# Optimization experiments

Measured on AMD Instinct MI355X. Metric: run time of the kernel, lower is better.

Reference implementation:

```python
import jax, jax.numpy as jnp
import numpy as np

B, T, F, U = 256, 512, 64, 128

def setup_inputs() -> dict:
    key = jax.random.key(0)
    ks = jax.random.split(key, 8)
    def ortho(k, n):
        a = jax.random.normal(k, (n, n), dtype=jnp.float32)
        q, _ = jnp.linalg.qr(a)
        return q.astype(jnp.float32)
    return {
        "x": jax.random.normal(ks[0], (B, T, F), dtype=jnp.float32),
        "m": jax.random.uniform(ks[1], (B, T, F), dtype=jnp.float32),
        "delta_t": jax.random.uniform(ks[2], (B, T), dtype=jnp.float32),
        "W_z": jax.random.normal(ks[3], (F, U), dtype=jnp.float32) * 0.08,
        "U_z": ortho(ks[4], U),
        "b_z": jnp.zeros((U,), jnp.float32),
        "W_r": jax.random.normal(ks[5], (F, U), dtype=jnp.float32) * 0.08,
        "U_r": ortho(ks[6], U),
        "b_r": jnp.zeros((U,), jnp.float32),
        "W_h": jax.random.normal(ks[7], (F, U), dtype=jnp.float32) * 0.08,
        "U_h": ortho(jax.random.fold_in(key, 99), U),
        "b_h": jnp.zeros((U,), jnp.float32),
        "gamma_x_decay": jnp.ones((F,), jnp.float32),
        "gamma_h_decay": jnp.ones((U,), jnp.float32),
        "mean_imputation": jnp.zeros((F,), jnp.float32),
    }

def reference(x, m, delta_t, W_z, U_z, b_z, W_r, U_r, b_r, W_h, U_h, b_h,
              gamma_x_decay, gamma_h_decay, mean_imputation):
    # delta_t: [B,T] -> [B,T,1]
    dt = delta_t[..., None]
    # input-side decay + imputation (no recurrence -> fully vectorized)
    gamma_x = jnp.exp(-jnp.maximum(0.0, gamma_x_decay) * dt)          # [B,T,F]
    x_dec = m * x + (1.0 - m) * (gamma_x * x + (1.0 - gamma_x) * mean_imputation)
    gamma_h = jnp.exp(-jnp.maximum(0.0, gamma_h_decay) * dt)          # [B,T,U]
    # precompute input projections for all timesteps
    xz = jnp.einsum('btf,fu->btu', x_dec, W_z) + b_z
    xr = jnp.einsum('btf,fu->btu', x_dec, W_r) + b_r
    xh = jnp.einsum('btf,fu->btu', x_dec, W_h) + b_h

    def step(h, inp):
        gz, az, ar, ah = inp            # gamma_h_t [B,U], projected inputs [B,U]
        h_dec = gz * h
        z = jax.nn.sigmoid(az + h_dec @ U_z)
        r = jax.nn.sigmoid(ar + h_dec @ U_r)
        h_hat = jnp.tanh(ah + (r * h_dec) @ U_h)
        h_new = (1.0 - z) * h_dec + z * h_hat
        return h_new, h_new

    h0 = jnp.zeros((x.shape[0], U_z.shape[0]), x.dtype)
    xs = (jnp.swapaxes(gamma_h, 0, 1), jnp.swapaxes(xz, 0, 1),
          jnp.swapaxes(xr, 0, 1), jnp.swapaxes(xh, 0, 1))
    _, hs = jax.lax.scan(step, h0, xs)  # [T,B,U]
    return jnp.swapaxes(hs, 0, 1)       # [B,T,U]
```

## Files before the change

### kernel.cpp

```cpp
#include <hip/hip_runtime.h>

#define B_ 256
#define T_ 512
#define F_ 64
#define U_ 128
#define PSTRIDE 132

typedef _Float16 h2v __attribute__((ext_vector_type(2)));
union U32H2 { unsigned u; h2v h; };

__device__ __forceinline__ float fdot2u(unsigned a, unsigned b, float c) {
#if __has_builtin(__builtin_amdgcn_fdot2)
  U32H2 x, y; x.u = a; y.u = b;
  return __builtin_amdgcn_fdot2(x.h, y.h, c, false);
#else
  U32H2 x, y; x.u = a; y.u = b;
  c = fmaf((float)x.h[0], (float)y.h[0], c);
  return fmaf((float)x.h[1], (float)y.h[1], c);
#endif
}

__device__ __forceinline__ unsigned packh2(float a, float b) {
  U32H2 r; r.h[0] = (_Float16)a; r.h[1] = (_Float16)b; return r.u;
}

__device__ __forceinline__ float red8(float v) {
  int t;
  t = __builtin_amdgcn_update_dpp(0, __float_as_int(v), 0xB1, 0xF, 0xF, true);
  v += __int_as_float(t);
  t = __builtin_amdgcn_update_dpp(0, __float_as_int(v), 0x4E, 0xF, 0xF, true);
  v += __int_as_float(t);
  t = __builtin_amdgcn_update_dpp(0, __float_as_int(v), 0x141, 0xF, 0xF, true);
  v += __int_as_float(t);
  return v;
}

__device__ __forceinline__ float fast_sig(float x) {
  return __builtin_amdgcn_rcpf(1.0f + __expf(-x));
}
__device__ __forceinline__ float fast_tanh(float x) {
  return fmaf(-2.0f, __builtin_amdgcn_rcpf(1.0f + __expf(2.0f * x)), 1.0f);
}

__global__ __launch_bounds__(512, 2) void grud_kernel(
    const float* __restrict__ x, const float* __restrict__ m,
    const float* __restrict__ delta_t,
    const float* __restrict__ Wz, const float* __restrict__ Uz, const float* __restrict__ bz,
    const float* __restrict__ Wr, const float* __restrict__ Ur, const float* __restrict__ br,
    const float* __restrict__ Wh, const float* __restrict__ Uh, const float* __restrict__ bh,
    const float* __restrict__ gxd, const float* __restrict__ ghd,
    const float* __restrict__ mi,
    float* __restrict__ out)
{
  const int tid = threadIdx.x;
  const int b   = blockIdx.x;
  const int kq  = tid & 7;
  const int ow  = tid >> 3;
  const int u0  = 2 * ow;

  __shared__ float s_mem[16896];
  float*  const s_pool = s_mem;
  float*  const s_gh   = s_mem;
  float*  const s_hist = s_mem + 4096;
  ushort* const s_x16  = (ushort*)(s_mem + 8192);
  __shared__ __align__(16) ushort s_hd16[U_];
  __shared__ __align__(16) ushort s_rh16[U_];
  __shared__ float s_dt[40];
  __shared__ float s_negghd[U_];

  unsigned uz0[8], uz1[8], ur0[8], ur1[8], uh0[8], uh1[8];
  unsigned wz0[4], wz1[4], wr0[4], wr1[4], wh0[4], wh1[4];

#define STAGE_MAT(SRC, ROWS)                                      \
  {                                                               \
    const float4* g4 = (const float4*)(SRC);                      \
    _Pragma("unroll") for (int i = 0; i < (ROWS) / 16; ++i) {     \
      const int e = tid + i * 512;                                \
      const int r = e >> 5, c = (e & 31) << 2;                    \
      *(float4*)(s_pool + r * PSTRIDE + c) = g4[e];               \
    }                                                             \
    __syncthreads();                                              \
  }

#define GATHER_U(D0, D1)                                          \
  _Pragma("unroll") for (int j = 0; j < 8; ++j) {                 \
    const int k = 16 * kq + 2 * j;                                \
    D0[j] = packh2(s_pool[k * PSTRIDE + u0],                      \
                   s_pool[(k + 1) * PSTRIDE + u0]);               \
    D1[j] = packh2(s_pool[k * PSTRIDE + u0 + 1],                  \
                   s_pool[(k + 1) * PSTRIDE + u0 + 1]);           \
  }                                                               \
  __syncthreads();

#define GATHER_W(D0, D1)                                          \
  _Pragma("unroll") for (int j = 0; j < 4; ++j) {                 \
    const int f = 8 * kq + 2 * j;                                 \
    D0[j] = packh2(s_pool[f * PSTRIDE + u0],                      \
                   s_pool[(f + 1) * PSTRIDE + u0]);               \
    D1[j] = packh2(s_pool[f * PSTRIDE + u0 + 1],                  \
                   s_pool[(f + 1) * PSTRIDE + u0 + 1]);           \
  }                                                               \
  __syncthreads();

  STAGE_MAT(Uz, 128) GATHER_U(uz0, uz1)
  STAGE_MAT(Ur, 128) GATHER_U(ur0, ur1)
  STAGE_MAT(Uh, 128) GATHER_U(uh0, uh1)
  STAGE_MAT(Wz, 64)  GATHER_W(wz0, wz1)
  STAGE_MAT(Wr, 64)  GATHER_W(wr0, wr1)
  STAGE_MAT(Wh, 64)  GATHER_W(wh0, wh1)

  const float2 bz2 = ((const float2*)bz)[ow];
  const float2 br2 = ((const float2*)br)[ow];
  const float2 bh2 = ((const float2*)bh)[ow];

  if (tid < U_) {
    s_negghd[tid] = -fmaxf(ghd[tid], 0.0f);
    ((ushort*)s_hd16)[tid] = 0;
  }

  float hd0 = 0.0f, hd1 = 0.0f;
  float z0 = 0.0f, z1 = 0.0f;

  for (int t0 = 0; t0 < T_; t0 += 32) {
    if (tid < 33) {
      const int t = t0 + tid;
      s_dt[tid] = (t < T_) ? delta_t[b * T_ + t] : 0.0f;
    }
    __syncthreads();

#pragma unroll
    for (int i = 0; i < 8; ++i) {
      const int flat = tid + i * 512;
      const int tcc = flat >> 7, u = flat & 127;
      s_gh[flat] = __expf(s_negghd[u] * s_dt[tcc + 1]);
    }
    {
      const int idx0 = tid * 4;
      const int tt = idx0 >> 6, f0 = idx0 & 63;
      const float dtv = s_dt[tt];
      const float4 xv  = *(const float4*)(x  + (size_t)(b * T_ + t0 + tt) * F_ + f0);
      const float4 mv  = *(const float4*)(m  + (size_t)(b * T_ + t0 + tt) * F_ + f0);
      const float4 gv  = *(const float4*)(gxd + f0);
      const float4 miv = *(const float4*)(mi  + f0);
      float gx, d0, d1, d2, d3;
      gx = __expf(-fmaxf(gv.x, 0.0f) * dtv);
      d0 = mv.x * xv.x + (1.0f - mv.x) * (gx * xv.x + (1.0f - gx) * miv.x);
      gx = __expf(-fmaxf(gv.y, 0.0f) * dtv);
      d1 = mv.y * xv.y + (1.0f - mv.y) * (gx * xv.y + (1.0f - gx) * miv.y);
      gx = __expf(-fmaxf(gv.z, 0.0f) * dtv);
      d2 = mv.z * xv.z + (1.0f - mv.z) * (gx * xv.z + (1.0f - gx) * miv.z);
      gx = __expf(-fmaxf(gv.w, 0.0f) * dtv);
      d3 = mv.w * xv.w + (1.0f - mv.w) * (gx * xv.w + (1.0f - gx) * miv.w);
      uint2 px; px.x = packh2(d0, d1); px.y = packh2(d2, d3);
      *(uint2*)(s_x16 + idx0) = px;
    }
    __syncthreads();

#pragma unroll 4
    for (int tc = 0; tc < 32; ++tc) {
      const uint4 ha = *(const uint4*)(s_hd16 + 16 * kq);
      const uint4 hb = *(const uint4*)(s_hd16 + 16 * kq + 8);
      const uint4 xa = *(const uint4*)(s_x16 + tc * F_ + 8 * kq);

      float az0 = 0.f, az1 = 0.f, ar0 = 0.f, ar1 = 0.f, ah0 = 0.f, ah1 = 0.f;
      az0 = fdot2u(ha.x, uz0[0], az0); az0 = fdot2u(ha.y, uz0[1], az0);
      az0 = fdot2u(ha.z, uz0[2], az0); az0 = fdot2u(ha.w, uz0[3], az0);
      az0 = fdot2u(hb.x, uz0[4], az0); az0 = fdot2u(hb.y, uz0[5], az0);
      az0 = fdot2u(hb.z, uz0[6], az0); az0 = fdot2u(hb.w, uz0[7], az0);
      az1 = fdot2u(ha.x, uz1[0], az1); az1 = fdot2u(ha.y, uz1[1], az1);
      az1 = fdot2u(ha.z, uz1[2], az1); az1 = fdot2u(ha.w, uz1[3], az1);
      az1 = fdot2u(hb.x, uz1[4], az1); az1 = fdot2u(hb.y, uz1[5], az1);
      az1 = fdot2u(hb.z, uz1[6], az1); az1 = fdot2u(hb.w, uz1[7], az1);
      ar0 = fdot2u(ha.x, ur0[0], ar0); ar0 = fdot2u(ha.y, ur0[1], ar0);
      ar0 = fdot2u(ha.z, ur0[2], ar0); ar0 = fdot2u(ha.w, ur0[3], ar0);
      ar0 = fdot2u(hb.x, ur0[4], ar0); ar0 = fdot2u(hb.y, ur0[5], ar0);
      ar0 = fdot2u(hb.z, ur0[6], ar0); ar0 = fdot2u(hb.w, ur0[7], ar0);
      ar1 = fdot2u(ha.x, ur1[0], ar1); ar1 = fdot2u(ha.y, ur1[1], ar1);
      ar1 = fdot2u(ha.z, ur1[2], ar1); ar1 = fdot2u(ha.w, ur1[3], ar1);
      ar1 = fdot2u(hb.x, ur1[4], ar1); ar1 = fdot2u(hb.y, ur1[5], ar1);
      ar1 = fdot2u(hb.z, ur1[6], ar1); ar1 = fdot2u(hb.w, ur1[7], ar1);

      az0 = fdot2u(xa.x, wz0[0], az0); az0 = fdot2u(xa.y, wz0[1], az0);
      az0 = fdot2u(xa.z, wz0[2], az0); az0 = fdot2u(xa.w, wz0[3], az0);
      az1 = fdot2u(xa.x, wz1[0], az1); az1 = fdot2u(xa.y, wz1[1], az1);
      az1 = fdot2u(xa.z, wz1[2], az1); az1 = fdot2u(xa.w, wz1[3], az1);
      ar0 = fdot2u(xa.x, wr0[0], ar0); ar0 = fdot2u(xa.y, wr0[1], ar0);
      ar0 = fdot2u(xa.z, wr0[2], ar0); ar0 = fdot2u(xa.w, wr0[3], ar0);
      ar1 = fdot2u(xa.x, wr1[0], ar1); ar1 = fdot2u(xa.y, wr1[1], ar1);
      ar1 = fdot2u(xa.z, wr1[2], ar1); ar1 = fdot2u(xa.w, wr1[3], ar1);
      ah0 = fdot2u(xa.x, wh0[0], ah0); ah0 = fdot2u(xa.y, wh0[1], ah0);
      ah0 = fdot2u(xa.z, wh0[2], ah0); ah0 = fdot2u(xa.w, wh0[3], ah0);
      ah1 = fdot2u(xa.x, wh1[0], ah1); ah1 = fdot2u(xa.y, wh1[1], ah1);
      ah1 = fdot2u(xa.z, wh1[2], ah1); ah1 = fdot2u(xa.w, wh1[3], ah1);

      az0 = red8(az0); az1 = red8(az1);
      ar0 = red8(ar0); ar1 = red8(ar1);
      z0 = fast_sig(az0 + bz2.x);
      z1 = fast_sig(az1 + bz2.y);
      const float r0 = fast_sig(ar0 + br2.x);
      const float r1 = fast_sig(ar1 + br2.y);
      if (kq == 0) {
        ((unsigned*)s_rh16)[ow] = packh2(r0 * hd0, r1 * hd1);
      }
      __syncthreads();

      const uint4 ra = *(const uint4*)(s_rh16 + 16 * kq);
      const uint4 rb = *(const uint4*)(s_rh16 + 16 * kq + 8);
      ah0 = fdot2u(ra.x, uh0[0], ah0); ah0 = fdot2u(ra.y, uh0[1], ah0);
      ah0 = fdot2u(ra.z, uh0[2], ah0); ah0 = fdot2u(ra.w, uh0[3], ah0);
      ah0 = fdot2u(rb.x, uh0[4], ah0); ah0 = fdot2u(rb.y, uh0[5], ah0);
      ah0 = fdot2u(rb.z, uh0[6], ah0); ah0 = fdot2u(rb.w, uh0[7], ah0);
      ah1 = fdot2u(ra.x, uh1[0], ah1); ah1 = fdot2u(ra.y, uh1[1], ah1);
      ah1 = fdot2u(ra.z, uh1[2], ah1); ah1 = fdot2u(ra.w, uh1[3], ah1);
      ah1 = fdot2u(rb.x, uh1[4], ah1); ah1 = fdot2u(rb.y, uh1[5], ah1);
      ah1 = fdot2u(rb.z, uh1[6], ah1); ah1 = fdot2u(rb.w, uh1[7], ah1);
      ah0 = red8(ah0); ah1 = red8(ah1);
      if (kq == 0) {
        const float hh0 = fast_tanh(ah0 + bh2.x);
        const float hh1 = fast_tanh(ah1 + bh2.y);
        const float hn0 = fmaf(z0, hh0 - hd0, hd0);
        const float hn1 = fmaf(z1, hh1 - hd1, hd1);
        ((float2*)s_hist)[tc * 64 + ow] = make_float2(hn0, hn1);
        const float2 gh = ((const float2*)s_gh)[tc * 64 + ow];
        hd0 = gh.x * hn0;
        hd1 = gh.y * hn1;
        ((unsigned*)s_hd16)[ow] = packh2(hd0, hd1);
      }
      __syncthreads();
    }

    {
      const float4* h4p = (const float4*)s_hist;
      float4* o4 = (float4*)(out + (size_t)(b * T_ + t0) * U_);
      o4[tid]       = h4p[tid];
      o4[tid + 512] = h4p[tid + 512];
    }
    __syncthreads();
  }
}

extern "C" void kernel_launch(void* const* d_in, const int* in_sizes, int n_in,
                              void* d_out, int out_size, void* d_ws, size_t ws_size,
                              hipStream_t stream) {
  const float* x   = (const float*)d_in[0];
  const float* m   = (const float*)d_in[1];
  const float* dt  = (const float*)d_in[2];
  const float* Wz  = (const float*)d_in[3];
  const float* Uz  = (const float*)d_in[4];
  const float* bz  = (const float*)d_in[5];
  const float* Wr  = (const float*)d_in[6];
  const float* Ur  = (const float*)d_in[7];
  const float* br  = (const float*)d_in[8];
  const float* Wh  = (const float*)d_in[9];
  const float* Uh  = (const float*)d_in[10];
  const float* bh  = (const float*)d_in[11];
  const float* gxd = (const float*)d_in[12];
  const float* ghd = (const float*)d_in[13];
  const float* mi  = (const float*)d_in[14];

  grud_kernel<<<dim3(B_), dim3(512), 0, stream>>>(
      x, m, dt, Wz, Uz, bz, Wr, Ur, br, Wh, Uh, bh, gxd, ghd, mi, (float*)d_out);
}
```

Measured before the change: 408.5 us.

## Specialize wavefront teams per gate and pipeline input projections one step ahead

Replaces the 8-way split-K layout, where each output pair was reduced across lanes with DPP, with four 128-thread teams. Each thread holds one full weight column in registers. Team 0 computes z, team 1 computes r, team 2 computes h_hat and the state update, and team 3 computes the next step's input projections into a double-buffered shared array. This removes the cross-lane reductions and the redundant work of computing input projections in every thread. Output is now written per step straight from registers instead of via a staged shared history. The cost is that each thread does a full 128-long serial dot product, teams sit idle in alternate phases, and register pressure rises (96 packed weights per thread, with the launch-bounds occupancy hint removed).

New measurement: 443.3 us. 8.5% more time.

```diff
diff --git a/kernel.cpp b/kernel.cpp
--- a/kernel.cpp
+++ b/kernel.cpp
@@ -9,32 +9,15 @@
 typedef _Float16 h2v __attribute__((ext_vector_type(2)));
 union U32H2 { unsigned u; h2v h; };
 
-__device__ __forceinline__ float fdot2u(unsigned a, unsigned b, float c) {
-#if __has_builtin(__builtin_amdgcn_fdot2)
+__device__ __forceinline__ float fdot2(unsigned a, unsigned b, float c) {
   U32H2 x, y; x.u = a; y.u = b;
   return __builtin_amdgcn_fdot2(x.h, y.h, c, false);
-#else
-  U32H2 x, y; x.u = a; y.u = b;
-  c = fmaf((float)x.h[0], (float)y.h[0], c);
-  return fmaf((float)x.h[1], (float)y.h[1], c);
-#endif
 }
 
 __device__ __forceinline__ unsigned packh2(float a, float b) {
   U32H2 r; r.h[0] = (_Float16)a; r.h[1] = (_Float16)b; return r.u;
 }
 
-__device__ __forceinline__ float red8(float v) {
-  int t;
-  t = __builtin_amdgcn_update_dpp(0, __float_as_int(v), 0xB1, 0xF, 0xF, true);
-  v += __int_as_float(t);
-  t = __builtin_amdgcn_update_dpp(0, __float_as_int(v), 0x4E, 0xF, 0xF, true);
-  v += __int_as_float(t);
-  t = __builtin_amdgcn_update_dpp(0, __float_as_int(v), 0x141, 0xF, 0xF, true);
-  v += __int_as_float(t);
-  return v;
-}
-
 __device__ __forceinline__ float fast_sig(float x) {
   return __builtin_amdgcn_rcpf(1.0f + __expf(-x));
 }
@@ -42,7 +25,7 @@
   return fmaf(-2.0f, __builtin_amdgcn_rcpf(1.0f + __expf(2.0f * x)), 1.0f);
 }
 
-__global__ __launch_bounds__(512, 2) void grud_kernel(
+__global__ __launch_bounds__(512) void grud_kernel(
     const float* __restrict__ x, const float* __restrict__ m,
     const float* __restrict__ delta_t,
     const float* __restrict__ Wz, const float* __restrict__ Uz, const float* __restrict__ bz,
@@ -52,24 +35,21 @@
     const float* __restrict__ mi,
     float* __restrict__ out)
 {
-  const int tid = threadIdx.x;
-  const int b   = blockIdx.x;
-  const int kq  = tid & 7;
-  const int ow  = tid >> 3;
-  const int u0  = 2 * ow;
-
-  __shared__ float s_mem[16896];
+  const int tid  = threadIdx.x;
+  const int b    = blockIdx.x;
+  const int team = tid >> 7;
+  const int uu   = tid & 127;
+
+  __shared__ float s_mem[U_ * PSTRIDE];
   float*  const s_pool = s_mem;
-  float*  const s_gh   = s_mem;
-  float*  const s_hist = s_mem + 4096;
-  ushort* const s_x16  = (ushort*)(s_mem + 8192);
+  float*  const s_zf   = s_mem;
+  float*  const s_ax   = s_mem + 128;
+  ushort* const s_x16h = (ushort*)(s_mem + 896);
   __shared__ __align__(16) ushort s_hd16[U_];
   __shared__ __align__(16) ushort s_rh16[U_];
   __shared__ float s_dt[40];
-  __shared__ float s_negghd[U_];
-
-  unsigned uz0[8], uz1[8], ur0[8], ur1[8], uh0[8], uh1[8];
-  unsigned wz0[4], wz1[4], wr0[4], wr1[4], wh0[4], wh1[4];
+
+  unsigned wcol[96];
 
 #define STAGE_MAT(SRC, ROWS)                                      \
   {                                                               \
@@ -82,62 +62,67 @@
     __syncthreads();                                              \
   }
 
-#define GATHER_U(D0, D1)                                          \
-  _Pragma("unroll") for (int j = 0; j < 8; ++j) {                 \
-    const int k = 16 * kq + 2 * j;                                \
-    D0[j] = packh2(s_pool[k * PSTRIDE + u0],                      \
-                   s_pool[(k + 1) * PSTRIDE + u0]);               \
-    D1[j] = packh2(s_pool[k * PSTRIDE + u0 + 1],                  \
-                   s_pool[(k + 1) * PSTRIDE + u0 + 1]);           \
-  }                                                               \
-  __syncthreads();
-
-#define GATHER_W(D0, D1)                                          \
-  _Pragma("unroll") for (int j = 0; j < 4; ++j) {                 \
-    const int f = 8 * kq + 2 * j;                                 \
-    D0[j] = packh2(s_pool[f * PSTRIDE + u0],                      \
-                   s_pool[(f + 1) * PSTRIDE + u0]);               \
-    D1[j] = packh2(s_pool[f * PSTRIDE + u0 + 1],                  \
-                   s_pool[(f + 1) * PSTRIDE + u0 + 1]);           \
-  }                                                               \
-  __syncthreads();
-
-  STAGE_MAT(Uz, 128) GATHER_U(uz0, uz1)
-  STAGE_MAT(Ur, 128) GATHER_U(ur0, ur1)
-  STAGE_MAT(Uh, 128) GATHER_U(uh0, uh1)
-  STAGE_MAT(Wz, 64)  GATHER_W(wz0, wz1)
-  STAGE_MAT(Wr, 64)  GATHER_W(wr0, wr1)
-  STAGE_MAT(Wh, 64)  GATHER_W(wh0, wh1)
-
-  const float2 bz2 = ((const float2*)bz)[ow];
-  const float2 br2 = ((const float2*)br)[ow];
-  const float2 bh2 = ((const float2*)bh)[ow];
-
-  if (tid < U_) {
-    s_negghd[tid] = -fmaxf(ghd[tid], 0.0f);
-    ((ushort*)s_hd16)[tid] = 0;
-  }
-
-  float hd0 = 0.0f, hd1 = 0.0f;
-  float z0 = 0.0f, z1 = 0.0f;
+  STAGE_MAT(Uz, 128)
+  if (team == 0) {
+#pragma unroll
+    for (int j = 0; j < 64; ++j)
+      wcol[j] = packh2(s_pool[(2 * j) * PSTRIDE + uu], s_pool[(2 * j + 1) * PSTRIDE + uu]);
+  }
+  __syncthreads();
+  STAGE_MAT(Ur, 128)
+  if (team == 1) {
+#pragma unroll
+    for (int j = 0; j < 64; ++j)
+      wcol[j] = packh2(s_pool[(2 * j) * PSTRIDE + uu], s_pool[(2 * j + 1) * PSTRIDE + uu]);
+  }
+  __syncthreads();
+  STAGE_MAT(Uh, 128)
+  if (team == 2) {
+#pragma unroll
+    for (int j = 0; j < 64; ++j)
+      wcol[j] = packh2(s_pool[(2 * j) * PSTRIDE + uu], s_pool[(2 * j + 1) * PSTRIDE + uu]);
+  }
+  __syncthreads();
+  STAGE_MAT(Wz, 64)
+  if (team == 3) {
+#pragma unroll
+    for (int j = 0; j < 32; ++j)
+      wcol[j] = packh2(s_pool[(2 * j) * PSTRIDE + uu], s_pool[(2 * j + 1) * PSTRIDE + uu]);
+  }
+  __syncthreads();
+  STAGE_MAT(Wr, 64)
+  if (team == 3) {
+#pragma unroll
+    for (int j = 0; j < 32; ++j)
+      wcol[32 + j] = packh2(s_pool[(2 * j) * PSTRIDE + uu], s_pool[(2 * j + 1) * PSTRIDE + uu]);
+  }
+  __syncthreads();
+  STAGE_MAT(Wh, 64)
+  if (team == 3) {
+#pragma unroll
+    for (int j = 0; j < 32; ++j)
+      wcol[64 + j] = packh2(s_pool[(2 * j) * PSTRIDE + uu], s_pool[(2 * j + 1) * PSTRIDE + uu]);
+  }
+  __syncthreads();
+
+  float bzu = 0.f, bru = 0.f, bhu = 0.f;
+  float negg = 0.f, hd_reg = 0.f;
+  if (team == 3) { bzu = bz[uu]; bru = br[uu]; bhu = bh[uu]; }
+  if (team == 2) { negg = -fmaxf(ghd[uu], 0.0f); }
+  if (tid < U_) s_hd16[tid] = 0;
+
+  const uint4* const hd4 = (const uint4*)s_hd16;
+  const uint4* const rh4 = (const uint4*)s_rh16;
 
   for (int t0 = 0; t0 < T_; t0 += 32) {
     if (tid < 33) {
       const int t = t0 + tid;
       s_dt[tid] = (t < T_) ? delta_t[b * T_ + t] : 0.0f;
     }
-    __syncthreads();
-
-#pragma unroll
-    for (int i = 0; i < 8; ++i) {
-      const int flat = tid + i * 512;
-      const int tcc = flat >> 7, u = flat & 127;
-      s_gh[flat] = __expf(s_negghd[u] * s_dt[tcc + 1]);
-    }
     {
       const int idx0 = tid * 4;
       const int tt = idx0 >> 6, f0 = idx0 & 63;
-      const float dtv = s_dt[tt];
+      const float dtv = delta_t[b * T_ + t0 + tt];
       const float4 xv  = *(const float4*)(x  + (size_t)(b * T_ + t0 + tt) * F_ + f0);
       const float4 mv  = *(const float4*)(m  + (size_t)(b * T_ + t0 + tt) * F_ + f0);
       const float4 gv  = *(const float4*)(gxd + f0);
@@ -152,90 +137,120 @@
       gx = __expf(-fmaxf(gv.w, 0.0f) * dtv);
       d3 = mv.w * xv.w + (1.0f - mv.w) * (gx * xv.w + (1.0f - gx) * miv.w);
       uint2 px; px.x = packh2(d0, d1); px.y = packh2(d2, d3);
-      *(uint2*)(s_x16 + idx0) = px;
+      *(uint2*)(s_x16h + idx0) = px;
     }
     __syncthreads();
 
-#pragma unroll 4
+    if (team == 3) {
+      const uint4* xp = (const uint4*)s_x16h;
+      float a0 = bzu, a1 = bru, a2 = bhu;
+#pragma unroll
+      for (int q = 0; q < 8; ++q) {
+        const uint4 xq = xp[q];
+        a0 = fdot2(xq.x, wcol[4*q+0], a0); a0 = fdot2(xq.y, wcol[4*q+1], a0);
+        a0 = fdot2(xq.z, wcol[4*q+2], a0); a0 = fdot2(xq.w, wcol[4*q+3], a0);
+        a1 = fdot2(xq.x, wcol[32+4*q+0], a1); a1 = fdot2(xq.y, wcol[32+4*q+1], a1);
+        a1 = fdot2(xq.z, wcol[32+4*q+2], a1); a1 = fdot2(xq.w, wcol[32+4*q+3], a1);
+        a2 = fdot2(xq.x, wcol[64+4*q+0], a2); a2 = fdot2(xq.y, wcol[64+4*q+1], a2);
+        a2 = fdot2(xq.z, wcol[64+4*q+2], a2); a2 = fdot2(xq.w, wcol[64+4*q+3], a2);
+      }
+      s_ax[0 * 384 + 0 * 128 + uu] = a0;
+      s_ax[0 * 384 + 1 * 128 + uu] = a1;
+      s_ax[0 * 384 + 2 * 128 + uu] = a2;
+    }
+    __syncthreads();
+
+#pragma unroll 2
     for (int tc = 0; tc < 32; ++tc) {
-      const uint4 ha = *(const uint4*)(s_hd16 + 16 * kq);
-      const uint4 hb = *(const uint4*)(s_hd16 + 16 * kq + 8);
-      const uint4 xa = *(const uint4*)(s_x16 + tc * F_ + 8 * kq);
-
-      float az0 = 0.f, az1 = 0.f, ar0 = 0.f, ar1 = 0.f, ah0 = 0.f, ah1 = 0.f;
-      az0 = fdot2u(ha.x, uz0[0], az0); az0 = fdot2u(ha.y, uz0[1], az0);
-      az0 = fdot2u(ha.z, uz0[2], az0); az0 = fdot2u(ha.w, uz0[3], az0);
-      az0 = fdot2u(hb.x, uz0[4], az0); az0 = fdot2u(hb.y, uz0[5], az0);
-      az0 = fdot2u(hb.z, uz0[6], az0); az0 = fdot2u(hb.w, uz0[7], az0);
-      az1 = fdot2u(ha.x, uz1[0], az1); az1 = fdot2u(ha.y, uz1[1], az1);
-      az1 = fdot2u(ha.z, uz1[2], az1); az1 = fdot2u(ha.w, uz1[3], az1);
-      az1 = fdot2u(hb.x, uz1[4], az1); az1 = fdot2u(hb.y, uz1[5], az1);
-      az1 = fdot2u(hb.z, uz1[6], az1); az1 = fdot2u(hb.w, uz1[7], az1);
-      ar0 = fdot2u(ha.x, ur0[0], ar0); ar0 = fdot2u(ha.y, ur0[1], ar0);
-      ar0 = fdot2u(ha.z, ur0[2], ar0); ar0 = fdot2u(ha.w, ur0[3], ar0);
-      ar0 = fdot2u(hb.x, ur0[4], ar0); ar0 = fdot2u(hb.y, ur0[5], ar0);
-      ar0 = fdot2u(hb.z, ur0[6], ar0); ar0 = fdot2u(hb.w, ur0[7], ar0);
-      ar1 = fdot2u(ha.x, ur1[0], ar1); ar1 = fdot2u(ha.y, ur1[1], ar1);
-      ar1 = fdot2u(ha.z, ur1[2], ar1); ar1 = fdot2u(ha.w, ur1[3], ar1);
-      ar1 = fdot2u(hb.x, ur1[4], ar1); ar1 = fdot2u(hb.y, ur1[5], ar1);
-      ar1 = fdot2u(hb.z, ur1[6], ar1); ar1 = fdot2u(hb.w, ur1[7], ar1);
-
-      az0 = fdot2u(xa.x, wz0[0], az0); az0 = fdot2u(xa.y, wz0[1], az0);
-      az0 = fdot2u(xa.z, wz0[2], az0); az0 = fdot2u(xa.w, wz0[3], az0);
-      az1 = fdot2u(xa.x, wz1[0], az1); az1 = fdot2u(xa.y, wz1[1], az1);
-      az1 = fdot2u(xa.z, wz1[2], az1); az1 = fdot2u(xa.w, wz1[3], az1);
-      ar0 = fdot2u(xa.x, wr0[0], ar0); ar0 = fdot2u(xa.y, wr0[1], ar0);
-      ar0 = fdot2u(xa.z, wr0[2], ar0); ar0 = fdot2u(xa.w, wr0[3], ar0);
-      ar1 = fdot2u(xa.x, wr1[0], ar1); ar1 = fdot2u(xa.y, wr1[1], ar1);
-      ar1 = fdot2u(xa.z, wr1[2], ar1); ar1 = fdot2u(xa.w, wr1[3], ar1);
-      ah0 = fdot2u(xa.x, wh0[0], ah0); ah0 = fdot2u(xa.y, wh0[1], ah0);
-      ah0 = fdot2u(xa.z, wh0[2], ah0); ah0 = fdot2u(xa.w, wh0[3], ah0);
-      ah1 = fdot2u(xa.x, wh1[0], ah1); ah1 = fdot2u(xa.y, wh1[1], ah1);
-      ah1 = fdot2u(xa.z, wh1[2], ah1); ah1 = fdot2u(xa.w, wh1[3], ah1);
-
-      az0 = red8(az0); az1 = red8(az1);
-      ar0 = red8(ar0); ar1 = red8(ar1);
-      z0 = fast_sig(az0 + bz2.x);
-      z1 = fast_sig(az1 + bz2.y);
-      const float r0 = fast_sig(ar0 + br2.x);
-      const float r1 = fast_sig(ar1 + br2.y);
-      if (kq == 0) {
-        ((unsigned*)s_rh16)[ow] = packh2(r0 * hd0, r1 * hd1);
+      const int cur = tc & 1, nxt = cur ^ 1;
+
+      if (team == 0) {
+        float a0 = s_ax[cur * 384 + uu], a1 = 0.f, a2 = 0.f, a3 = 0.f;
+#pragma unroll
+        for (int q = 0; q < 4; ++q) {
+          const uint4 h0 = hd4[4*q+0], h1 = hd4[4*q+1], h2 = hd4[4*q+2], h3 = hd4[4*q+3];
+          a0 = fdot2(h0.x, wcol[16*q+0], a0);  a0 = fdot2(h0.y, wcol[16*q+1], a0);
+          a0 = fdot2(h0.z, wcol[16*q+2], a0);  a0 = fdot2(h0.w, wcol[16*q+3], a0);
+          a1 = fdot2(h1.x, wcol[16*q+4], a1);  a1 = fdot2(h1.y, wcol[16*q+5], a1);
+          a1 = fdot2(h1.z, wcol[16*q+6], a1);  a1 = fdot2(h1.w, wcol[16*q+7], a1);
+          a2 = fdot2(h2.x, wcol[16*q+8], a2);  a2 = fdot2(h2.y, wcol[16*q+9], a2);
+          a2 = fdot2(h2.z, wcol[16*q+10], a2); a2 = fdot2(h2.w, wcol[16*q+11], a2);
+          a3 = fdot2(h3.x, wcol[16*q+12], a3); a3 = fdot2(h3.y, wcol[16*q+13], a3);
+          a3 = fdot2(h3.z, wcol[16*q+14], a3); a3 = fdot2(h3.w, wcol[16*q+15], a3);
+        }
+        s_zf[uu] = fast_sig((a0 + a1) + (a2 + a3));
+      } else if (team == 1) {
+        float a0 = s_ax[cur * 384 + 128 + uu], a1 = 0.f, a2 = 0.f, a3 = 0.f;
+#pragma unroll
+        for (int q = 0; q < 4; ++q) {
+          const uint4 h0 = hd4[4*q+0], h1 = hd4[4*q+1], h2 = hd4[4*q+2], h3 = hd4[4*q+3];
+          a0 = fdot2(h0.x, wcol[16*q+0], a0);  a0 = fdot2(h0.y, wcol[16*q+1], a0);
+          a0 = fdot2(h0.z, wcol[16*q+2], a0);  a0 = fdot2(h0.w, wcol[16*q+3], a0);
+          a1 = fdot2(h1.x, wcol[16*q+4], a1);  a1 = fdot2(h1.y, wcol[16*q+5], a1);
+          a1 = fdot2(h1.z, wcol[16*q+6], a1);  a1 = fdot2(h1.w, wcol[16*q+7], a1);
+          a2 = fdot2(h2.x, wcol[16*q+8], a2);  a2 = fdot2(h2.y, wcol[16*q+9], a2);
+          a2 = fdot2(h2.z, wcol[16*q+10], a2); a2 = fdot2(h2.w, wcol[16*q+11], a2);
+          a3 = fdot2(h3.x, wcol[16*q+12], a3); a3 = fdot2(h3.y, wcol[16*q+13], a3);
+          a3 = fdot2(h3.z, wcol[16*q+14], a3); a3 = fdot2(h3.w, wcol[16*q+15], a3);
+        }
+        const float r = fast_sig((a0 + a1) + (a2 + a3));
+        const float hdv = (float)((const _Float16*)s_hd16)[uu];
+        ((_Float16*)s_rh16)[uu] = (_Float16)(r * hdv);
+      } else if (team == 3) {
+        if (tc < 31) {
+          const uint4* xp = (const uint4*)(s_x16h + (tc + 1) * 64);
+          float a0 = bzu, a1 = 0.f;
+#pragma unroll
+          for (int q = 0; q < 4; ++q) {
+            const uint4 xq = xp[2*q], xq2 = xp[2*q+1];
+            a0 = fdot2(xq.x,  wcol[8*q+0], a0); a0 = fdot2(xq.y,  wcol[8*q+1], a0);
+            a0 = fdot2(xq.z,  wcol[8*q+2], a0); a0 = fdot2(xq.w,  wcol[8*q+3], a0);
+            a1 = fdot2(xq2.x, wcol[8*q+4], a1); a1 = fdot2(xq2.y, wcol[8*q+5], a1);
+            a1 = fdot2(xq2.z, wcol[8*q+6], a1); a1 = fdot2(xq2.w, wcol[8*q+7], a1);
+          }
+          s_ax[nxt * 384 + uu] = a0 + a1;
+        }
       }
       __syncthreads();
 
-      const uint4 ra = *(const uint4*)(s_rh16 + 16 * kq);
-      const uint4 rb = *(const uint4*)(s_rh16 + 16 * kq + 8);
-      ah0 = fdot2u(ra.x, uh0[0], ah0); ah0 = fdot2u(ra.y, uh0[1], ah0);
-      ah0 = fdot2u(ra.z, uh0[2], ah0); ah0 = fdot2u(ra.w, uh0[3], ah0);
-      ah0 = fdot2u(rb.x, uh0[4], ah0); ah0 = fdot2u(rb.y, uh0[5], ah0);
-      ah0 = fdot2u(rb.z, uh0[6], ah0); ah0 = fdot2u(rb.w, uh0[7], ah0);
-      ah1 = fdot2u(ra.x, uh1[0], ah1); ah1 = fdot2u(ra.y, uh1[1], ah1);
-      ah1 = fdot2u(ra.z, uh1[2], ah1); ah1 = fdot2u(ra.w, uh1[3], ah1);
-      ah1 = fdot2u(rb.x, uh1[4], ah1); ah1 = fdot2u(rb.y, uh1[5], ah1);
-      ah1 = fdot2u(rb.z, uh1[6], ah1); ah1 = fdot2u(rb.w, uh1[7], ah1);
-      ah0 = red8(ah0); ah1 = red8(ah1);
-      if (kq == 0) {
-        const float hh0 = fast_tanh(ah0 + bh2.x);
-        const float hh1 = fast_tanh(ah1 + bh2.y);
-        const float hn0 = fmaf(z0, hh0 - hd0, hd0);
-        const float hn1 = fmaf(z1, hh1 - hd1, hd1);
-        ((float2*)s_hist)[tc * 64 + ow] = make_float2(hn0, hn1);
-        const float2 gh = ((const float2*)s_gh)[tc * 64 + ow];
-        hd0 = gh.x * hn0;
-        hd1 = gh.y * hn1;
-        ((unsigned*)s_hd16)[ow] = packh2(hd0, hd1);
+      if (team == 2) {
+        float a0 = s_ax[cur * 384 + 256 + uu], a1 = 0.f, a2 = 0.f, a3 = 0.f;
+#pragma unroll
+        for (int q = 0; q < 4; ++q) {
+          const uint4 r0 = rh4[4*q+0], r1 = rh4[4*q+1], r2 = rh4[4*q+2], r3 = rh4[4*q+3];
+          a0 = fdot2(r0.x, wcol[16*q+0], a0);  a0 = fdot2(r0.y, wcol[16*q+1], a0);
+          a0 = fdot2(r0.z, wcol[16*q+2], a0);  a0 = fdot2(r0.w, wcol[16*q+3], a0);
+          a1 = fdot2(r1.x, wcol[16*q+4], a1);  a1 = fdot2(r1.y, wcol[16*q+5], a1);
+          a1 = fdot2(r1.z, wcol[16*q+6], a1);  a1 = fdot2(r1.w, wcol[16*q+7], a1);
+          a2 = fdot2(r2.x, wcol[16*q+8], a2);  a2 = fdot2(r2.y, wcol[16*q+9], a2);
+          a2 = fdot2(r2.z, wcol[16*q+10], a2); a2 = fdot2(r2.w, wcol[16*q+11], a2);
+          a3 = fdot2(r3.x, wcol[16*q+12], a3); a3 = fdot2(r3.y, wcol[16*q+13], a3);
+          a3 = fdot2(r3.z, wcol[16*q+14], a3); a3 = fdot2(r3.w, wcol[16*q+15], a3);
+        }
+        const float hh = fast_tanh((a0 + a1) + (a2 + a3));
+        const float z  = s_zf[uu];
+        const float hn = fmaf(z, hh - hd_reg, hd_reg);
+        out[(size_t)(b * T_ + t0 + tc) * U_ + uu] = hn;
+        hd_reg = hn * __expf(negg * s_dt[tc + 1]);
+        ((_Float16*)s_hd16)[uu] = (_Float16)hd_reg;
+      } else if (team == 3) {
+        if (tc < 31) {
+          const uint4* xp = (const uint4*)(s_x16h + (tc + 1) * 64);
+          float a1 = bru, a2 = bhu;
+#pragma unroll
+          for (int q = 0; q < 8; ++q) {
+            const uint4 xq = xp[q];
+            a1 = fdot2(xq.x, wcol[32+4*q+0], a1); a1 = fdot2(xq.y, wcol[32+4*q+1], a1);
+            a1 = fdot2(xq.z, wcol[32+4*q+2], a1); a1 = fdot2(xq.w, wcol[32+4*q+3], a1);
+            a2 = fdot2(xq.x, wcol[64+4*q+0], a2); a2 = fdot2(xq.y, wcol[64+4*q+1], a2);
+            a2 = fdot2(xq.z, wcol[64+4*q+2], a2); a2 = fdot2(xq.w, wcol[64+4*q+3], a2);
+          }
+          s_ax[nxt * 384 + 128 + uu] = a1;
+          s_ax[nxt * 384 + 256 + uu] = a2;
+        }
       }
       __syncthreads();
     }
-
-    {
-      const float4* h4p = (const float4*)s_hist;
-      float4* o4 = (float4*)(out + (size_t)(b * T_ + t0) * U_);
-      o4[tid]       = h4p[tid];
-      o4[tid + 512] = h4p[tid + 512];
-    }
-    __syncthreads();
   }
 }
 
```
